# Kernel tuning notes

Measured on AMD Instinct MI355X. Metric: run time of the kernel, lower is better.

## Reference

```python
import jax, jax.numpy as jnp
import numpy as np

N_NODES = 50000
N_EDGES = 640000
IN_FEATS = 512
HID = 128
OUT_FEATS = 128
N_GRAPHS = 256


def setup_inputs() -> dict:
    key = jax.random.key(0)
    ks = jax.random.split(key, 7)
    x = jax.random.normal(ks[0], (N_NODES, IN_FEATS), dtype=jnp.float32)
    edge_index = jax.random.randint(ks[1], (2, N_EDGES), 0, N_NODES, dtype=jnp.int32)
    batch = jnp.sort(jax.random.randint(ks[2], (N_NODES,), 0, N_GRAPHS, dtype=jnp.int32))
    W1 = jax.random.normal(ks[3], (IN_FEATS, HID), dtype=jnp.float32) * (1.0 / np.sqrt(IN_FEATS))
    b1 = jnp.zeros((HID,), jnp.float32)
    W2 = jax.random.normal(ks[4], (HID, OUT_FEATS), dtype=jnp.float32) * (1.0 / np.sqrt(HID))
    b2 = jnp.zeros((OUT_FEATS,), jnp.float32)
    return {"x": x, "W1": W1, "b1": b1, "W2": W2, "b2": b2,
            "edge_index": edge_index, "batch": batch}


def reference(x, W1, b1, W2, b2, edge_index, batch):
    N = x.shape[0]
    loop = jnp.arange(N, dtype=edge_index.dtype)
    # PyG GCNConv default: add self-loops, symmetric deg^-1/2 normalization
    row = jnp.concatenate([edge_index[0], loop])  # source
    col = jnp.concatenate([edge_index[1], loop])  # target
    deg = jax.ops.segment_sum(jnp.ones_like(col, x.dtype), col, num_segments=N)
    dinv = jnp.where(deg > 0, jax.lax.rsqrt(deg), 0.0)
    norm = dinv[row] * dinv[col]  # [E+N]

    def gcn_conv(h, W, b):
        h = h @ W  # linear transform first (PyG order)
        msg = h[row] * norm[:, None]  # gather + scale
        agg = jax.ops.segment_sum(msg, col, num_segments=N)  # scatter-add
        return agg + b

    h = jax.nn.relu(gcn_conv(x, W1, b1))  # dropout is identity in eval mode
    h = gcn_conv(h, W2, b2)
    hs = jax.ops.segment_sum(h, batch, num_segments=N_GRAPHS)  # global_add_pool
    return hs, h
```

## Files before the change

kernel.cpp:

```cpp
#include <hip/hip_runtime.h>
#include <hip/hip_bf16.h>

#define N_NODES  50000
#define N_EDGES  640000
#define IN_FEATS 512
#define HID      128
#define OUT_FEATS 128
#define N_GRAPHS 256

#define SCAN_CHUNK 1024
#define SCAN_BLOCKS ((N_NODES + SCAN_CHUNK - 1) / SCAN_CHUNK)

typedef __attribute__((ext_vector_type(8))) short short8;
typedef __attribute__((ext_vector_type(4))) float f32x4;

__device__ __forceinline__ float bf2f(unsigned u16) {
    return __uint_as_float(u16 << 16);
}
__device__ __forceinline__ unsigned short f2bf(float f) {
    __hip_bfloat16 h = __float2bfloat16(f);
    return *(unsigned short*)&h;
}

#define PREP_BLOCKS 644

__global__ __launch_bounds__(256) void k_prep(const float* __restrict__ W1,
                                              const float* __restrict__ W2,
                                              unsigned short* __restrict__ wt1,
                                              unsigned short* __restrict__ wt2,
                                              int* __restrict__ cnt,
                                              float* __restrict__ hs) {
    int b = blockIdx.x;
    int t = threadIdx.x;
    if (b < 196) {
        int i = b * 256 + t;
        if (i < N_NODES) cnt[i] = 0;
    } else if (b < 452) {
        int idx = (b - 196) * 256 + t;
        int n = idx & 127, k = idx >> 7;
        wt1[(size_t)n * IN_FEATS + k] = f2bf(W1[(size_t)k * 128 + n]);
    } else if (b < 516) {
        int idx = (b - 452) * 256 + t;
        int n = idx & 127, k = idx >> 7;
        wt2[(size_t)n * HID + k] = f2bf(W2[(size_t)k * 128 + n]);
    } else {
        int idx = (b - 516) * 256 + t;
        hs[idx] = 0.f;
    }
}


template <int K>
__global__ __launch_bounds__(256, 3) void k_g1c(const float* __restrict__ A,
                                                const unsigned short* __restrict__ Bt,
                                                unsigned short* __restrict__ Cb, int M,
                                                const int* __restrict__ col,
                                                int* __restrict__ cnt, int nblk_gemm) {
    int tid = threadIdx.x;

    if (blockIdx.x >= nblk_gemm) {
        int e4 = ((blockIdx.x - nblk_gemm) * 256 + tid) * 4;
        if (e4 < N_EDGES) {
            int4 c = *(const int4*)(col + e4);
            atomicAdd(&cnt[c.x], 1);
            atomicAdd(&cnt[c.y], 1);
            atomicAdd(&cnt[c.z], 1);
            atomicAdd(&cnt[c.w], 1);
        }
        return;
    }

    int wave = tid >> 6;
    int lane = tid & 63;
    int quad = lane >> 4;
    int l15 = lane & 15;
    int m0 = blockIdx.x * 64 + wave * 16;

    int row = m0 + l15;
    if (row >= M) row = M - 1;
    const float* ap = A + (size_t)row * K + quad * 8;
    const unsigned short* bp = Bt + (size_t)l15 * K + quad * 8;

    f32x4 acc[8];
#pragma unroll
    for (int nt = 0; nt < 8; ++nt) acc[nt] = (f32x4){0.f, 0.f, 0.f, 0.f};

    float4 a0 = *(const float4*)(ap);
    float4 a1 = *(const float4*)(ap + 4);
    short8 bcur[8];
#pragma unroll
    for (int nt = 0; nt < 8; ++nt)
        bcur[nt] = *(const short8*)(bp + (size_t)nt * 16 * K);

#pragma unroll 1
    for (int k0 = 0; k0 < K - 32; k0 += 32) {
        float4 na0 = *(const float4*)(ap + k0 + 32);
        float4 na1 = *(const float4*)(ap + k0 + 36);
        short8 bn[8];
#pragma unroll
        for (int nt = 0; nt < 8; ++nt)
            bn[nt] = *(const short8*)(bp + (size_t)nt * 16 * K + k0 + 32);

        short8 af;
        af[0] = (short)f2bf(a0.x); af[1] = (short)f2bf(a0.y);
        af[2] = (short)f2bf(a0.z); af[3] = (short)f2bf(a0.w);
        af[4] = (short)f2bf(a1.x); af[5] = (short)f2bf(a1.y);
        af[6] = (short)f2bf(a1.z); af[7] = (short)f2bf(a1.w);
#pragma unroll
        for (int nt = 0; nt < 8; ++nt)
            acc[nt] = __builtin_amdgcn_mfma_f32_16x16x32_bf16(af, bcur[nt], acc[nt], 0, 0, 0);

        a0 = na0; a1 = na1;
#pragma unroll
        for (int nt = 0; nt < 8; ++nt) bcur[nt] = bn[nt];
    }
    {
        short8 af;
        af[0] = (short)f2bf(a0.x); af[1] = (short)f2bf(a0.y);
        af[2] = (short)f2bf(a0.z); af[3] = (short)f2bf(a0.w);
        af[4] = (short)f2bf(a1.x); af[5] = (short)f2bf(a1.y);
        af[6] = (short)f2bf(a1.z); af[7] = (short)f2bf(a1.w);
#pragma unroll
        for (int nt = 0; nt < 8; ++nt)
            acc[nt] = __builtin_amdgcn_mfma_f32_16x16x32_bf16(af, bcur[nt], acc[nt], 0, 0, 0);
    }

#pragma unroll
    for (int nt = 0; nt < 8; ++nt) {
        int colb = nt * 16 + l15;
#pragma unroll
        for (int r2 = 0; r2 < 4; ++r2) {
            int gm = m0 + quad * 4 + r2;
            if (gm < M) Cb[(size_t)gm * 128 + colb] = f2bf(acc[nt][r2]);
        }
    }
}


__global__ __launch_bounds__(256) void k_scan_a(const int* __restrict__ cnt,
                                                int* __restrict__ offs,
                                                int* __restrict__ bsum) {
    __shared__ int sums[256];
    int t = threadIdx.x;
    int base = blockIdx.x * SCAN_CHUNK + t * 4;
    int c0 = 0, c1 = 0, c2 = 0, c3 = 0;
    if (base + 3 < N_NODES) {
        int4 v = *(const int4*)(cnt + base);
        c0 = v.x; c1 = v.y; c2 = v.z; c3 = v.w;
    } else {
        if (base + 0 < N_NODES) c0 = cnt[base + 0];
        if (base + 1 < N_NODES) c1 = cnt[base + 1];
        if (base + 2 < N_NODES) c2 = cnt[base + 2];
    }
    int ts = c0 + c1 + c2 + c3;
    sums[t] = ts;
    __syncthreads();
#pragma unroll
    for (int off = 1; off < 256; off <<= 1) {
        int add = (t >= off) ? sums[t - off] : 0;
        __syncthreads();
        sums[t] += add;
        __syncthreads();
    }
    int ex = sums[t] - ts;
    if (base + 3 < N_NODES) {
        int4 o;
        o.x = ex; o.y = ex + c0; o.z = ex + c0 + c1; o.w = ex + c0 + c1 + c2;
        *(int4*)(offs + base) = o;
    } else {
        if (base + 0 < N_NODES) offs[base + 0] = ex;
        if (base + 1 < N_NODES) offs[base + 1] = ex + c0;
        if (base + 2 < N_NODES) offs[base + 2] = ex + c0 + c1;
    }
    if (t == 255) bsum[blockIdx.x] = sums[255];
}

__global__ __launch_bounds__(256) void k_scan_c(const int* __restrict__ cnt,
                                                const int* __restrict__ bsum,
                                                int* __restrict__ offs,
                                                int* __restrict__ cursor,
                                                float* __restrict__ dinv) {
    __shared__ int sb[64];
    int t = threadIdx.x;
    int b = blockIdx.x;
    if (t < 64) sb[t] = (t < SCAN_BLOCKS) ? bsum[t] : 0;
    __syncthreads();
#pragma unroll
    for (int off = 1; off < 64; off <<= 1) {
        int add = 0;
        if (t < 64 && t >= off) add = sb[t - off];
        __syncthreads();
        if (t < 64) sb[t] += add;
        __syncthreads();
    }
    int add = (b == 0) ? 0 : sb[b - 1];
    int base = b * SCAN_CHUNK + t * 4;
    if (base + 3 < N_NODES) {
        int4 o = *(const int4*)(offs + base);
        o.x += add; o.y += add; o.z += add; o.w += add;
        *(int4*)(offs + base) = o;
        *(int4*)(cursor + base) = o;
        int4 c = *(const int4*)(cnt + base);
        float4 d;
        d.x = rsqrtf((float)c.x + 1.0f);
        d.y = rsqrtf((float)c.y + 1.0f);
        d.z = rsqrtf((float)c.z + 1.0f);
        d.w = rsqrtf((float)c.w + 1.0f);
        *(float4*)(dinv + base) = d;
    } else {
#pragma unroll
        for (int j = 0; j < 4; ++j) {
            int i = base + j;
            if (i < N_NODES) {
                int o = offs[i] + add;
                offs[i] = o; cursor[i] = o;
                dinv[i] = rsqrtf((float)cnt[i] + 1.0f);
            }
        }
    }
    if (b == 0 && t == 0) offs[N_NODES] = N_EDGES;
}

__global__ void k_fill(const int* __restrict__ row, const int* __restrict__ col,
                       int* __restrict__ cursor, int* __restrict__ srcIdx) {
    int e4 = (blockIdx.x * blockDim.x + threadIdx.x) * 4;
    if (e4 >= N_EDGES) return;
    int4 r = *(const int4*)(row + e4);
    int4 c = *(const int4*)(col + e4);
    srcIdx[atomicAdd(&cursor[c.x], 1)] = r.x;
    srcIdx[atomicAdd(&cursor[c.y], 1)] = r.y;
    srcIdx[atomicAdd(&cursor[c.z], 1)] = r.z;
    srcIdx[atomicAdd(&cursor[c.w], 1)] = r.w;
}


template <int RELU>
__global__ __launch_bounds__(256) void k_agg(const unsigned* __restrict__ t,
                                             const int* __restrict__ offs,
                                             const int* __restrict__ srcIdx,
                                             const float* __restrict__ dinv,
                                             const float* __restrict__ bias,
                                             unsigned* __restrict__ out_) {
    int wave = threadIdx.x >> 6;
    int lane = threadIdx.x & 63;
    int h = lane >> 5;
    int l = lane & 31;
    int i = blockIdx.x * 4 + wave;
    float di = dinv[i];
    const unsigned* my = t + (size_t)i * 64 + 2 * l;

    float s0 = 0.f, s1 = 0.f, s2 = 0.f, s3 = 0.f;
    {
        uint2 sv = *(const uint2*)my;
        if (h == 0) {
            s0 = bf2f(sv.x & 0xffffu) * di;
            s1 = bf2f(sv.x >> 16) * di;
            s2 = bf2f(sv.y & 0xffffu) * di;
            s3 = bf2f(sv.y >> 16) * di;
        }
    }
    int lo = offs[i], hi = offs[i + 1];
    for (int e = lo; e < hi; e += 16) {
        int idx[8];
        float d[8];
        uint2 v[8];
#pragma unroll
        for (int j = 0; j < 8; ++j) {
            int ee = e + 2 * j + h;
            idx[j] = (ee < hi) ? srcIdx[ee] : i;
        }
#pragma unroll
        for (int j = 0; j < 8; ++j)
            v[j] = *(const uint2*)(t + (size_t)idx[j] * 64 + 2 * l);
#pragma unroll
        for (int j = 0; j < 8; ++j) {
            int ee = e + 2 * j + h;
            d[j] = (ee < hi) ? dinv[idx[j]] : 0.f;
        }
#pragma unroll
        for (int j = 0; j < 8; ++j) {
            s0 = fmaf(bf2f(v[j].x & 0xffffu), d[j], s0);
            s1 = fmaf(bf2f(v[j].x >> 16),     d[j], s1);
            s2 = fmaf(bf2f(v[j].y & 0xffffu), d[j], s2);
            s3 = fmaf(bf2f(v[j].y >> 16),     d[j], s3);
        }
    }
    s0 += __shfl_xor(s0, 32);
    s1 += __shfl_xor(s1, 32);
    s2 += __shfl_xor(s2, 32);
    s3 += __shfl_xor(s3, 32);

    float r0 = s0 * di, r1 = s1 * di, r2 = s2 * di, r3 = s3 * di;
    if (bias) {
        float4 bb = *(const float4*)(bias + 4 * l);
        r0 += bb.x; r1 += bb.y; r2 += bb.z; r3 += bb.w;
    }
    if (RELU) {
        r0 = fmaxf(r0, 0.f); r1 = fmaxf(r1, 0.f);
        r2 = fmaxf(r2, 0.f); r3 = fmaxf(r3, 0.f);
    }
    if (h == 0) {
        uint2 o;
        o.x = (unsigned)f2bf(r0) | ((unsigned)f2bf(r1) << 16);
        o.y = (unsigned)f2bf(r2) | ((unsigned)f2bf(r3) << 16);
        *(uint2*)(out_ + (size_t)i * 64 + 2 * l) = o;
    }
}


__global__ __launch_bounds__(256) void k_gemm2_pool(const unsigned short* __restrict__ G,
                                                    const unsigned short* __restrict__ Bt,
                                                    const float* __restrict__ bias,
                                                    const int* __restrict__ batch,
                                                    float* __restrict__ out,
                                                    float* __restrict__ hs, int M) {
    const int K = HID;
    __shared__ unsigned short As[4][64][8];
    __shared__ unsigned short Bs[4][128][8];
    int tid = threadIdx.x;
    int wave = tid >> 6;
    int lane = tid & 63;
    int quad = lane >> 4;
    int l15 = lane & 15;
    int m0 = blockIdx.x * 64;

    f32x4 acc[8];
#pragma unroll
    for (int nt = 0; nt < 8; ++nt) acc[nt] = (f32x4){0.f, 0.f, 0.f, 0.f};

    int gm_a = m0 + lane; if (gm_a >= M) gm_a = M - 1;
    const unsigned short* ap_base = G + (size_t)gm_a * K + wave * 8;

    for (int k0 = 0; k0 < K; k0 += 32) {
        *(short8*)&As[wave][lane][0] = *(const short8*)(ap_base + k0);
#pragma unroll
        for (int i = 0; i < 2; ++i) {
            int slot = tid + i * 256;
            int bkq = slot >> 7;
            int n = slot & 127;
            *(short8*)&Bs[bkq][n][0] = *(const short8*)(Bt + (size_t)n * K + k0 + bkq * 8);
        }
        __syncthreads();
        short8 a = *(short8*)&As[quad][wave * 16 + l15][0];
#pragma unroll
        for (int nt = 0; nt < 8; ++nt) {
            short8 b = *(short8*)&Bs[quad][nt * 16 + l15][0];
            acc[nt] = __builtin_amdgcn_mfma_f32_16x16x32_bf16(a, b, acc[nt], 0, 0, 0);
        }
        __syncthreads();
    }
    int rb = m0 + wave * 16 + quad * 4;
    int g_[4];
#pragma unroll
    for (int r2 = 0; r2 < 4; ++r2)
        g_[r2] = (rb + r2 < M) ? batch[rb + r2] : -1;
#pragma unroll
    for (int nt = 0; nt < 8; ++nt) {
        int colb = nt * 16 + l15;
        float bcol = bias[colb];
        float v[4];
#pragma unroll
        for (int r2 = 0; r2 < 4; ++r2) {
            v[r2] = acc[nt][r2] + bcol;
            if (rb + r2 < M) out[(size_t)(rb + r2) * 128 + colb] = v[r2];
        }
        float run = v[0];
        int gcur = g_[0];
#pragma unroll
        for (int r2 = 1; r2 < 4; ++r2) {
            if (g_[r2] == gcur) run += v[r2];
            else {
                if (gcur >= 0) atomicAdd(&hs[(size_t)gcur * 128 + colb], run);
                gcur = g_[r2]; run = v[r2];
            }
        }
        if (gcur >= 0) atomicAdd(&hs[(size_t)gcur * 128 + colb], run);
    }
}


extern "C" void kernel_launch(void* const* d_in, const int* in_sizes, int n_in,
                              void* d_out, int out_size, void* d_ws, size_t ws_size,
                              hipStream_t stream) {
    const float* x  = (const float*)d_in[0];
    const float* W1 = (const float*)d_in[1];
    const float* b1 = (const float*)d_in[2];
    const float* W2 = (const float*)d_in[3];
    const float* b2 = (const float*)d_in[4];
    const int*   ei = (const int*)d_in[5];
    const int*   batch = (const int*)d_in[6];
    const int* row = ei;
    const int* col = ei + N_EDGES;

    float* out_hs = (float*)d_out;
    float* out_h  = (float*)d_out + N_GRAPHS * OUT_FEATS;

    char* ws = (char*)d_ws;
    unsigned short* tb   = (unsigned short*)ws;
    unsigned short* h1b  = (unsigned short*)(ws + 12800000);
    unsigned short* gb   = (unsigned short*)(ws + 25600000);
    float* dinv = (float*)(ws + 38400000);
    int*   cnt    = (int*)(ws + 38600000);
    int*   offs   = (int*)(ws + 38800000);
    int*   cursor = (int*)(ws + 39000016);
    int*   srcIdx = (int*)(ws + 39200016);
    int*   bsum   = (int*)(ws + 41761056);
    unsigned short* wt1 = (unsigned short*)(ws + 41761472);
    unsigned short* wt2 = (unsigned short*)(ws + 41892544);

    const int TB = 256;
    const int GB1 = (N_NODES + 63) / 64;
    const int CB  = (N_EDGES / 4 + TB - 1) / TB;

    k_prep<<<PREP_BLOCKS, 256, 0, stream>>>(W1, W2, wt1, wt2, cnt, out_hs);
    k_g1c<IN_FEATS><<<GB1 + CB, 256, 0, stream>>>(x, wt1, tb, N_NODES, col, cnt, GB1);
    k_scan_a<<<SCAN_BLOCKS, 256, 0, stream>>>(cnt, offs, bsum);
    k_scan_c<<<SCAN_BLOCKS, 256, 0, stream>>>(cnt, bsum, offs, cursor, dinv);
    k_fill<<<(N_EDGES / 4 + TB - 1) / TB, TB, 0, stream>>>(row, col, cursor, srcIdx);

    k_agg<1><<<N_NODES / 4, 256, 0, stream>>>((const unsigned*)tb, offs, srcIdx, dinv, b1, (unsigned*)h1b);
    k_agg<0><<<N_NODES / 4, 256, 0, stream>>>((const unsigned*)h1b, offs, srcIdx, dinv, nullptr, (unsigned*)gb);
    k_gemm2_pool<<<(N_NODES + 63) / 64, 256, 0, stream>>>(gb, wt2, b2, batch, out_h, out_hs, N_NODES);
}
```

Measured before the change: 351.6 us.

## Split GEMM1 N-dimension across waves and double-buffer K loop loads

Each wave now computes a 16x64 output tile (half the columns) instead of 16x128, doubling the number of waves and halving accumulator and B registers per wave. This allows raising launch bounds occupancy from 3 to 4 blocks per CU. The K loop is unrolled by two with two in-flight load stages and scheduling barriers to overlap global loads with MFMA. Each A row is now read twice (once per column half), adding read traffic on the fp32 input. The M-tail guard is dropped, which relies on N_NODES being divisible by 16.

```diff
diff --git a/kernel.cpp b/kernel.cpp
--- a/kernel.cpp
+++ b/kernel.cpp
@@ -50,8 +50,17 @@
 }
 
 
+__device__ __forceinline__ short8 cvt8(float4 x, float4 y) {
+    short8 r;
+    r[0] = (short)f2bf(x.x); r[1] = (short)f2bf(x.y);
+    r[2] = (short)f2bf(x.z); r[3] = (short)f2bf(x.w);
+    r[4] = (short)f2bf(y.x); r[5] = (short)f2bf(y.y);
+    r[6] = (short)f2bf(y.z); r[7] = (short)f2bf(y.w);
+    return r;
+}
+
 template <int K>
-__global__ __launch_bounds__(256, 3) void k_g1c(const float* __restrict__ A,
+__global__ __launch_bounds__(256, 4) void k_g1c(const float* __restrict__ A,
                                                 const unsigned short* __restrict__ Bt,
                                                 unsigned short* __restrict__ Cb, int M,
                                                 const int* __restrict__ col,
@@ -74,64 +83,74 @@
     int lane = tid & 63;
     int quad = lane >> 4;
     int l15 = lane & 15;
-    int m0 = blockIdx.x * 64 + wave * 16;
-
-    int row = m0 + l15;
-    if (row >= M) row = M - 1;
-    const float* ap = A + (size_t)row * K + quad * 8;
-    const unsigned short* bp = Bt + (size_t)l15 * K + quad * 8;
-
-    f32x4 acc[8];
-#pragma unroll
-    for (int nt = 0; nt < 8; ++nt) acc[nt] = (f32x4){0.f, 0.f, 0.f, 0.f};
-
-    float4 a0 = *(const float4*)(ap);
-    float4 a1 = *(const float4*)(ap + 4);
-    short8 bcur[8];
-#pragma unroll
-    for (int nt = 0; nt < 8; ++nt)
-        bcur[nt] = *(const short8*)(bp + (size_t)nt * 16 * K);
+    int unit = blockIdx.x * 4 + wave;
+    int nunits = (M >> 4) * 2;
+    if (unit >= nunits) return;
+    int s  = unit >> 1;
+    int ch = unit & 1;
+    int m0 = s * 16;
+
+    const float* ap = A + (size_t)(m0 + l15) * K + quad * 8;
+    const unsigned short* bp = Bt + (size_t)(ch * 64 + l15) * K + quad * 8;
+
+    f32x4 acc0 = (f32x4){0.f,0.f,0.f,0.f}, acc1 = acc0, acc2 = acc0, acc3 = acc0;
+
+#define LOADA(v0, v1, k)  { v0 = *(const float4*)(ap + (k)); v1 = *(const float4*)(ap + (k) + 4); }
+#define LOADB(b0, b1, b2, b3, k) { \
+    b0 = *(const short8*)(bp + (size_t)0 * 16 * K + (k)); \
+    b1 = *(const short8*)(bp + (size_t)1 * 16 * K + (k)); \
+    b2 = *(const short8*)(bp + (size_t)2 * 16 * K + (k)); \
+    b3 = *(const short8*)(bp + (size_t)3 * 16 * K + (k)); }
+#define MFMA4(af, b0, b1, b2, b3) { \
+    acc0 = __builtin_amdgcn_mfma_f32_16x16x32_bf16(af, b0, acc0, 0, 0, 0); \
+    acc1 = __builtin_amdgcn_mfma_f32_16x16x32_bf16(af, b1, acc1, 0, 0, 0); \
+    acc2 = __builtin_amdgcn_mfma_f32_16x16x32_bf16(af, b2, acc2, 0, 0, 0); \
+    acc3 = __builtin_amdgcn_mfma_f32_16x16x32_bf16(af, b3, acc3, 0, 0, 0); }
+
+    float4 aA0, aA1, aB0, aB1;
+    short8 bA0, bA1, bA2, bA3, bB0, bB1, bB2, bB3;
+    LOADA(aA0, aA1, 0); LOADB(bA0, bA1, bA2, bA3, 0);
+    LOADA(aB0, aB1, 32); LOADB(bB0, bB1, bB2, bB3, 32);
 
 #pragma unroll 1
-    for (int k0 = 0; k0 < K - 32; k0 += 32) {
-        float4 na0 = *(const float4*)(ap + k0 + 32);
-        float4 na1 = *(const float4*)(ap + k0 + 36);
-        short8 bn[8];
-#pragma unroll
-        for (int nt = 0; nt < 8; ++nt)
-            bn[nt] = *(const short8*)(bp + (size_t)nt * 16 * K + k0 + 32);
-
-        short8 af;
-        af[0] = (short)f2bf(a0.x); af[1] = (short)f2bf(a0.y);
-        af[2] = (short)f2bf(a0.z); af[3] = (short)f2bf(a0.w);
-        af[4] = (short)f2bf(a1.x); af[5] = (short)f2bf(a1.y);
-        af[6] = (short)f2bf(a1.z); af[7] = (short)f2bf(a1.w);
-#pragma unroll
-        for (int nt = 0; nt < 8; ++nt)
-            acc[nt] = __builtin_amdgcn_mfma_f32_16x16x32_bf16(af, bcur[nt], acc[nt], 0, 0, 0);
-
-        a0 = na0; a1 = na1;
-#pragma unroll
-        for (int nt = 0; nt < 8; ++nt) bcur[nt] = bn[nt];
+    for (int k0 = 0; k0 < K - 64; k0 += 64) {
+        {
+            float4 nA0, nA1; short8 nB0, nB1, nB2, nB3;
+            LOADA(nA0, nA1, k0 + 64); LOADB(nB0, nB1, nB2, nB3, k0 + 64);
+            __builtin_amdgcn_sched_barrier(0);
+            short8 af = cvt8(aA0, aA1);
+            MFMA4(af, bA0, bA1, bA2, bA3);
+            aA0 = nA0; aA1 = nA1;
+            bA0 = nB0; bA1 = nB1; bA2 = nB2; bA3 = nB3;
+        }
+        {
+            float4 mA0, mA1; short8 mB0, mB1, mB2, mB3;
+            LOADA(mA0, mA1, k0 + 96); LOADB(mB0, mB1, mB2, mB3, k0 + 96);
+            __builtin_amdgcn_sched_barrier(0);
+            short8 af = cvt8(aB0, aB1);
+            MFMA4(af, bB0, bB1, bB2, bB3);
+            aB0 = mA0; aB1 = mA1;
+            bB0 = mB0; bB1 = mB1; bB2 = mB2; bB3 = mB3;
+        }
     }
     {
-        short8 af;
-        af[0] = (short)f2bf(a0.x); af[1] = (short)f2bf(a0.y);
-        af[2] = (short)f2bf(a0.z); af[3] = (short)f2bf(a0.w);
-        af[4] = (short)f2bf(a1.x); af[5] = (short)f2bf(a1.y);
-        af[6] = (short)f2bf(a1.z); af[7] = (short)f2bf(a1.w);
-#pragma unroll
-        for (int nt = 0; nt < 8; ++nt)
-            acc[nt] = __builtin_amdgcn_mfma_f32_16x16x32_bf16(af, bcur[nt], acc[nt], 0, 0, 0);
-    }
-
-#pragma unroll
-    for (int nt = 0; nt < 8; ++nt) {
-        int colb = nt * 16 + l15;
+        short8 af = cvt8(aA0, aA1);
+        MFMA4(af, bA0, bA1, bA2, bA3);
+        af = cvt8(aB0, aB1);
+        MFMA4(af, bB0, bB1, bB2, bB3);
+    }
+#undef LOADA
+#undef LOADB
+#undef MFMA4
+
+    f32x4 accs[4] = {acc0, acc1, acc2, acc3};
+#pragma unroll
+    for (int nt = 0; nt < 4; ++nt) {
+        int colb = ch * 64 + nt * 16 + l15;
 #pragma unroll
         for (int r2 = 0; r2 < 4; ++r2) {
             int gm = m0 + quad * 4 + r2;
-            if (gm < M) Cb[(size_t)gm * 128 + colb] = f2bf(acc[nt][r2]);
+            Cb[(size_t)gm * 128 + colb] = f2bf(accs[nt][r2]);
         }
     }
 }
@@ -409,7 +428,8 @@
     unsigned short* wt2 = (unsigned short*)(ws + 41892544);
 
     const int TB = 256;
-    const int GB1 = (N_NODES + 63) / 64;
+    const int NUNITS = (N_NODES / 16) * 2;
+    const int GB1 = (NUNITS + 3) / 4;
     const int CB  = (N_EDGES / 4 + TB - 1) / TB;
 
     k_prep<<<PREP_BLOCKS, 256, 0, stream>>>(W1, W2, wt1, wt2, cnt, out_hs);
```

New measurement: 367.8 us. 1.05x slower.
